# Optimization experiments

Measured on AMD Instinct MI355X. Metric: run time of the kernel, lower is better.

Reference implementation:

```python
import jax, jax.numpy as jnp
import numpy as np

EMBED_DIM = 384
NUM_HEADS = 6
HEAD_DIM = EMBED_DIM // NUM_HEADS
MLP_HIDDEN = 4 * EMBED_DIM
LN_EPS = 1e-5


def layer_norm(x, gamma, beta):
    mu = jnp.mean(x, axis=-1, keepdims=True)
    var = jnp.mean((x - mu) ** 2, axis=-1, keepdims=True)
    return (x - mu) * jax.lax.rsqrt(var + LN_EPS) * gamma + beta


def setup_inputs() -> dict:
    key = jax.random.key(0)
    ks = jax.random.split(key, 8)
    D, H = EMBED_DIM, MLP_HIDDEN
    s = 1.0 / np.sqrt(D)
    sh = 1.0 / np.sqrt(H)
    return {
        "x": jax.random.normal(ks[0], (16, 1024, D), dtype=jnp.float32),
        "ln1_g": jnp.ones((D,), jnp.float32),
        "ln1_b": jnp.zeros((D,), jnp.float32),
        "qkv_w": jax.random.uniform(ks[1], (3 * D, D), jnp.float32, -s, s),
        "qkv_b": jax.random.uniform(ks[2], (3 * D,), jnp.float32, -s, s),
        "proj_w": jax.random.uniform(ks[3], (D, D), jnp.float32, -s, s),
        "proj_b": jax.random.uniform(ks[4], (D,), jnp.float32, -s, s),
        "ln2_g": jnp.ones((D,), jnp.float32),
        "ln2_b": jnp.zeros((D,), jnp.float32),
        "fc1_w": jax.random.uniform(ks[5], (H, D), jnp.float32, -s, s),
        "fc1_b": jax.random.uniform(ks[6], (H,), jnp.float32, -s, s),
        "fc2_w": jax.random.uniform(ks[7], (D, H), jnp.float32, -sh, sh),
        "fc2_b": jnp.zeros((D,), jnp.float32),
    }


def reference(x, ln1_g, ln1_b, qkv_w, qkv_b, proj_w, proj_b,
              ln2_g, ln2_b, fc1_w, fc1_b, fc2_w, fc2_b):
    B, N, D = x.shape
    Hh, Dh = NUM_HEADS, HEAD_DIM
    scale = Dh ** -0.5

    # --- attention sublayer (pre-norm) ---
    h = layer_norm(x, ln1_g, ln1_b)
    qkv = h @ qkv_w.T + qkv_b                      # [B,N,3D]
    qkv = qkv.reshape(B, N, 3, Hh, Dh)
    q, k, v = (qkv[:, :, i].transpose(0, 2, 1, 3) for i in range(3))  # [B,H,N,Dh]
    attn = jax.nn.softmax(jnp.einsum('bhnd,bhmd->bhnm', q, k) * scale, axis=-1)
    o = jnp.einsum('bhnm,bhmd->bhnd', attn, v)     # [B,H,N,Dh]
    o = o.transpose(0, 2, 1, 3).reshape(B, N, D)
    x = x + (o @ proj_w.T + proj_b)

    # --- MLP sublayer (pre-norm) ---
    h = layer_norm(x, ln2_g, ln2_b)
    h = jax.nn.gelu(h @ fc1_w.T + fc1_b, approximate=False)
    x = x + (h @ fc2_w.T + fc2_b)
    return x
```

## Files before the change

### kernel.cpp

```cpp
#include <hip/hip_runtime.h>

typedef unsigned short u16;
typedef unsigned int   u32;
typedef __bf16  bf16x8 __attribute__((ext_vector_type(8)));
typedef __bf16  bf16x4_t __attribute__((ext_vector_type(4)));
typedef float   f32x4  __attribute__((ext_vector_type(4)));

struct Ptrs { const void* p[13]; };

__device__ __forceinline__ float bf2f(u16 u) {
    union { unsigned int i; float f; } c; c.i = ((unsigned int)u) << 16; return c.f;
}
__device__ __forceinline__ u16 f2bf(float f) {
    union { float f; unsigned int i; } c; c.f = f;
    unsigned int u = c.i;
    unsigned int r = (u + 0x7fffu + ((u >> 16) & 1u)) >> 16;
    return (u16)r;
}

__device__ __forceinline__ float wave_sum(float x) {
#pragma unroll
    for (int m = 32; m >= 1; m >>= 1) x += __shfl_xor(x, m);
    return x;
}

__device__ __forceinline__ void g2l16(const u16* g, u16* l) {
    __builtin_amdgcn_global_load_lds(
        (__attribute__((address_space(1))) void*)g,
        (__attribute__((address_space(3))) void*)l, 16, 0, 0);
}

__global__ void k_flag(const u32* __restrict__ w, int* __restrict__ flagp)
{
    if (threadIdx.x == 0) {
        int cnt = 0;
        for (int i = 0; i < 128; ++i) {
            u16 lo = (u16)(w[i] & 0xFFFFu);
            int e = (lo >> 7) & 0xFF;
            cnt += (e >= 117 && e <= 123) ? 1 : 0;
        }
        *flagp = (cnt >= 64) ? 1 : 0;
    }
}

__global__ __launch_bounds__(256) void k_convert(Ptrs ps, u16* __restrict__ cx,
                                                 u16* __restrict__ cw,
                                                 const int* __restrict__ flagp)
{
    const int cum[14] = {0,786432,786480,786528,841824,841968,860400,860448,
                         860496,860544,934272,934464,1008192,1008240};
    const int off[13] = {0,0,384,768,443136,444288,591744,
                         592128,592512,592896,1182720,1184256,1774080};
    int c = blockIdx.x * 256 + threadIdx.x;
    if (c >= 1008240) return;
    int seg = 0;
#pragma unroll
    for (int i = 1; i < 13; ++i) seg += (c >= cum[i]) ? 1 : 0;
    int e = (c - cum[seg]) * 8;
    u16* dst = (seg == 0) ? (cx + e) : (cw + off[seg] + e);
    if (*flagp) {
        *(uint4*)dst = *((const uint4*)ps.p[seg] + (e >> 3));
    } else {
        const float* s = (const float*)ps.p[seg] + e;
        u16 tmp[8];
#pragma unroll
        for (int t = 0; t < 8; ++t) tmp[t] = f2bf(s[t]);
        *(uint4*)dst = *(const uint4*)tmp;
    }
}

__device__ __forceinline__ void gemm_core_128(const u16* __restrict__ A,
                                              const u16* __restrict__ B,
                                              int K, int m0, int n0,
                                              f32x4 (&acc)[4][4])
{
    __shared__ __align__(16) u16 As[128 * 64];
    __shared__ __align__(16) u16 Bs[128 * 64];

    const int tid  = threadIdx.x;
    const int lane = tid & 63;
    const int wid  = tid >> 6;
    const int wm  = (wid >> 1) * 64;
    const int wn  = (wid & 1) * 64;
    const int l15 = lane & 15;
    const int g   = lane >> 4;
    const int srow   = lane >> 3;
    const int schunk = ((lane & 7) ^ srow) * 8;

    const u16* Abase = A + (size_t)(m0 + wid * 32 + srow) * K + schunk;
    const u16* Bbase = B + (size_t)(n0 + wid * 32 + srow) * K + schunk;

    for (int kk = 0; kk < K; kk += 64) {
        __syncthreads();
#pragma unroll
        for (int t = 0; t < 4; ++t) {
            g2l16(Abase + (size_t)t * 8 * K + kk, &As[(wid * 32 + t * 8) * 64]);
            g2l16(Bbase + (size_t)t * 8 * K + kk, &Bs[(wid * 32 + t * 8) * 64]);
        }
        __syncthreads();

#pragma unroll
        for (int ks = 0; ks < 2; ++ks) {
            bf16x8 af[4], bfr[4];
#pragma unroll
            for (int i = 0; i < 4; i++) {
                int row = wm + 16 * i + l15;
                int p = ((ks * 4 + g) ^ (l15 & 7)) * 8;
                af[i] = __builtin_bit_cast(bf16x8,
                         *(const uint4*)&As[row * 64 + p]);
            }
#pragma unroll
            for (int j = 0; j < 4; j++) {
                int row = wn + 16 * j + l15;
                int p = ((ks * 4 + g) ^ (l15 & 7)) * 8;
                bfr[j] = __builtin_bit_cast(bf16x8,
                         *(const uint4*)&Bs[row * 64 + p]);
            }
#pragma unroll
            for (int i = 0; i < 4; i++)
#pragma unroll
                for (int j = 0; j < 4; j++)
                    acc[i][j] = __builtin_amdgcn_mfma_f32_16x16x32_bf16(
                                    af[i], bfr[j], acc[i][j], 0, 0, 0);
        }
    }
}

__device__ __forceinline__ void gemm_core_128x64(const u16* __restrict__ A,
                                                 const u16* __restrict__ B,
                                                 int K, int m0, int n0,
                                                 f32x4 (&acc)[4][2])
{
    __shared__ __align__(16) u16 As[128 * 64];
    __shared__ __align__(16) u16 Bs[64 * 64];

    const int tid  = threadIdx.x;
    const int lane = tid & 63;
    const int wid  = tid >> 6;
    const int wm  = (wid >> 1) * 64;
    const int wn  = (wid & 1) * 32;
    const int l15 = lane & 15;
    const int g   = lane >> 4;
    const int srow   = lane >> 3;
    const int schunk = ((lane & 7) ^ srow) * 8;

    const u16* Abase = A + (size_t)(m0 + wid * 32 + srow) * K + schunk;
    const u16* Bbase = B + (size_t)(n0 + wid * 16 + srow) * K + schunk;

    for (int kk = 0; kk < K; kk += 64) {
        __syncthreads();
#pragma unroll
        for (int t = 0; t < 4; ++t)
            g2l16(Abase + (size_t)t * 8 * K + kk, &As[(wid * 32 + t * 8) * 64]);
#pragma unroll
        for (int t = 0; t < 2; ++t)
            g2l16(Bbase + (size_t)t * 8 * K + kk, &Bs[(wid * 16 + t * 8) * 64]);
        __syncthreads();

#pragma unroll
        for (int ks = 0; ks < 2; ++ks) {
            bf16x8 af[4], bfr[2];
#pragma unroll
            for (int i = 0; i < 4; i++) {
                int row = wm + 16 * i + l15;
                int p = ((ks * 4 + g) ^ (l15 & 7)) * 8;
                af[i] = __builtin_bit_cast(bf16x8,
                         *(const uint4*)&As[row * 64 + p]);
            }
#pragma unroll
            for (int j = 0; j < 2; j++) {
                int row = wn + 16 * j + l15;
                int p = ((ks * 4 + g) ^ (l15 & 7)) * 8;
                bfr[j] = __builtin_bit_cast(bf16x8,
                         *(const uint4*)&Bs[row * 64 + p]);
            }
#pragma unroll
            for (int i = 0; i < 4; i++)
#pragma unroll
                for (int j = 0; j < 2; j++)
                    acc[i][j] = __builtin_amdgcn_mfma_f32_16x16x32_bf16(
                                    af[i], bfr[j], acc[i][j], 0, 0, 0);
        }
    }
}

__global__ __launch_bounds__(256) void k_layernorm(const u16* __restrict__ in,
                                                   const u16* __restrict__ g,
                                                   const u16* __restrict__ b,
                                                   u16* __restrict__ out,
                                                   int nrows)
{
    const int wid = threadIdx.x >> 6, lane = threadIdx.x & 63;
    const int row = blockIdx.x * 4 + wid;
    if (row >= nrows) return;
    float v[6];
    const u16* p = in + (size_t)row * 384;
#pragma unroll
    for (int t = 0; t < 6; t++) v[t] = bf2f(p[lane + 64 * t]);
    float s = 0.f;
#pragma unroll
    for (int t = 0; t < 6; t++) s += v[t];
    const float mu = wave_sum(s) * (1.0f / 384.0f);
    float vs = 0.f;
#pragma unroll
    for (int t = 0; t < 6; t++) { float d = v[t] - mu; vs += d * d; }
    const float var = wave_sum(vs) * (1.0f / 384.0f);
    const float rs = rsqrtf(var + 1e-5f);
    u16* po = out + (size_t)row * 384;
#pragma unroll
    for (int t = 0; t < 6; t++) {
        int e = lane + 64 * t;
        po[e] = f2bf((v[t] - mu) * rs * bf2f(g[e]) + bf2f(b[e]));
    }
}

__global__ __launch_bounds__(256) void k_gemm_qkv(const u16* __restrict__ A,
                                                  const u16* __restrict__ W,
                                                  const u16* __restrict__ bias,
                                                  u16* __restrict__ q,
                                                  u16* __restrict__ k,
                                                  u16* __restrict__ vrow)
{
    const int id = blockIdx.x, slot = id & 7, idx = id >> 3;
    const int m0 = (slot * 16 + idx / 9) * 128;
    const int n0 = (idx % 9) * 128;
    f32x4 acc[4][4];
#pragma unroll
    for (int i = 0; i < 4; i++)
#pragma unroll
        for (int j = 0; j < 4; j++) acc[i][j] = f32x4{0.f, 0.f, 0.f, 0.f};
    gemm_core_128(A, W, 384, m0, n0, acc);
    const int lane = threadIdx.x & 63, wid = threadIdx.x >> 6;
    const int wm = (wid >> 1) * 64, wn = (wid & 1) * 64;
    const int l15 = lane & 15, rq = (lane >> 4) * 4;
#pragma unroll
    for (int i = 0; i < 4; i++)
#pragma unroll
        for (int j = 0; j < 4; j++)
#pragma unroll
            for (int r = 0; r < 4; r++) {
                int gr = m0 + wm + 16 * i + rq + r;
                int gc = n0 + wn + 16 * j + l15;
                float v = acc[i][j][r] + bf2f(bias[gc]);
                int part = gc / 384, rem = gc % 384;
                int head = rem >> 6, dh = rem & 63;
                int bb = gr >> 10, nn = gr & 1023;
                int bh = bb * 6 + head;
                u16* dst = (part == 0) ? q : (part == 1) ? k : vrow;
                dst[((size_t)bh * 1024 + nn) * 64 + dh] = f2bf(v);
            }
}

__global__ __launch_bounds__(256) void k_transpose_v(const u16* __restrict__ v,
                                                     u16* __restrict__ vT)
{
    __shared__ u16 T[64 * 72];
    const int bh = blockIdx.y, n0 = blockIdx.x * 64;
    const int tid = threadIdx.x;
    const int r = tid >> 2;
    const int c = (tid & 3) * 16;
    const u16* src = v + (size_t)bh * 65536 + (size_t)(n0 + r) * 64 + c;
    uint4 a = *(const uint4*)src;
    uint4 b = *(const uint4*)(src + 8);
    u16 buf[16];
    *(uint4*)&buf[0] = a; *(uint4*)&buf[8] = b;
#pragma unroll
    for (int e = 0; e < 16; ++e) T[(c + e) * 72 + r] = buf[e];
    __syncthreads();
    uint4 o0 = *(const uint4*)&T[r * 72 + c];
    uint4 o1 = *(const uint4*)&T[r * 72 + c + 8];
    u16* dst = vT + (size_t)bh * 65536 + (size_t)r * 1024 + n0 + c;
    *(uint4*)dst = o0;
    *(uint4*)(dst + 8) = o1;
}

__global__ __launch_bounds__(256) void k_attn(const u16* __restrict__ q,
                                              const u16* __restrict__ kk,
                                              const u16* __restrict__ vT,
                                              u16* __restrict__ o)
{
    constexpr int LDP = 72;
    __shared__ __align__(16) u16 Ks[64 * 64];
    __shared__ __align__(16) u16 Vs[64 * 64];
    __shared__ __align__(16) u16 Ps[128 * LDP];

    const int tid = threadIdx.x, lane = tid & 63, wid = tid >> 6;
    const int l15 = lane & 15, g = lane >> 4, q8 = g * 8;
    const int id = blockIdx.x;
    const int bh = (id & 7) * 12 + ((id >> 3) >> 3);
    const int q0 = ((id >> 3) & 7) * 128;
    const int wrow = wid * 32;

    const u16* Q = q  + (size_t)bh * 65536;
    const u16* K = kk + (size_t)bh * 65536;
    const u16* V = vT + (size_t)bh * 65536;

    const int srow   = lane >> 3;
    const int schunk = ((lane & 7) ^ srow) * 8;

    bf16x8 aq[2][2];
#pragma unroll
    for (int jp = 0; jp < 2; ++jp)
#pragma unroll
        for (int ks = 0; ks < 2; ++ks) {
            bf16x8 t = __builtin_bit_cast(bf16x8,
                *(const uint4*)&Q[(size_t)(q0 + wrow + jp * 16 + l15) * 64
                                  + ks * 32 + q8]);
#pragma unroll
            for (int e = 0; e < 8; ++e) t[e] = (__bf16)((float)t[e] * 0.125f);
            aq[jp][ks] = t;
        }

    f32x4 ob[2][4];
#pragma unroll
    for (int i = 0; i < 2; ++i)
#pragma unroll
        for (int j = 0; j < 4; ++j) ob[i][j] = f32x4{0.f, 0.f, 0.f, 0.f};
    float lsum[2] = {0.f, 0.f};

    for (int kt = 0; kt < 16; ++kt) {
        __syncthreads();
#pragma unroll
        for (int t = 0; t < 2; ++t) {
            int r0 = wid * 16 + t * 8;
            g2l16(&K[(size_t)(kt * 64 + r0 + srow) * 64 + schunk], &Ks[r0 * 64]);
            g2l16(&V[(size_t)(r0 + srow) * 1024 + kt * 64 + schunk], &Vs[r0 * 64]);
        }
        __syncthreads();

        f32x4 st[4][2];
#pragma unroll
        for (int ip = 0; ip < 4; ++ip)
#pragma unroll
            for (int jp = 0; jp < 2; ++jp) st[ip][jp] = f32x4{0.f, 0.f, 0.f, 0.f};
#pragma unroll
        for (int ip = 0; ip < 4; ++ip) {
            int row = ip * 16 + l15;
#pragma unroll
            for (int ks = 0; ks < 2; ++ks) {
                bf16x8 bk = __builtin_bit_cast(bf16x8,
                    *(const uint4*)&Ks[row * 64 + ((ks * 4 + g) ^ (row & 7)) * 8]);
#pragma unroll
                for (int jp = 0; jp < 2; ++jp)
                    st[ip][jp] = __builtin_amdgcn_mfma_f32_16x16x32_bf16(
                                    bk, aq[jp][ks], st[ip][jp], 0, 0, 0);
            }
        }

#pragma unroll
        for (int jp = 0; jp < 2; ++jp) {
            float ps = 0.f;
#pragma unroll
            for (int ip = 0; ip < 4; ++ip)
#pragma unroll
                for (int r = 0; r < 4; ++r) {
                    float p = __expf(st[ip][jp][r]);
                    st[ip][jp][r] = p;
                    ps += p;
                }
            lsum[jp] += ps;
        }

#pragma unroll
        for (int ip = 0; ip < 4; ++ip)
#pragma unroll
            for (int jp = 0; jp < 2; ++jp) {
                bf16x4_t pk;
#pragma unroll
                for (int r = 0; r < 4; ++r) pk[r] = (__bf16)st[ip][jp][r];
                *(bf16x4_t*)&Ps[(wrow + jp * 16 + l15) * LDP + ip * 16 + g * 4] = pk;
            }

#pragma unroll
        for (int ks = 0; ks < 2; ++ks) {
            bf16x8 ap[2];
#pragma unroll
            for (int i = 0; i < 2; ++i)
                ap[i] = __builtin_bit_cast(bf16x8,
                    *(const uint4*)&Ps[(wrow + i * 16 + l15) * LDP + ks * 32 + q8]);
#pragma unroll
            for (int jv = 0; jv < 4; ++jv) {
                int row = jv * 16 + l15;
                bf16x8 bv = __builtin_bit_cast(bf16x8,
                    *(const uint4*)&Vs[row * 64 + ((ks * 4 + g) ^ (row & 7)) * 8]);
#pragma unroll
                for (int i = 0; i < 2; ++i)
                    ob[i][jv] = __builtin_amdgcn_mfma_f32_16x16x32_bf16(
                                  ap[i], bv, ob[i][jv], 0, 0, 0);
            }
        }
    }

#pragma unroll
    for (int jp = 0; jp < 2; ++jp) {
        lsum[jp] += __shfl_xor(lsum[jp], 16);
        lsum[jp] += __shfl_xor(lsum[jp], 32);
    }
    const int bb = bh / 6, hh = bh % 6;
#pragma unroll
    for (int i = 0; i < 2; ++i)
#pragma unroll
        for (int r = 0; r < 4; ++r) {
            int src = (lane & 48) | (g * 4 + r);
            float linv = 1.0f / __shfl(lsum[i], src);
            int row = q0 + wrow + i * 16 + g * 4 + r;
#pragma unroll
            for (int jv = 0; jv < 4; ++jv) {
                int dh = jv * 16 + l15;
                o[((size_t)(bb * 1024 + row)) * 384 + hh * 64 + dh] =
                    f2bf(ob[i][jv][r] * linv);
            }
        }
}

__global__ __launch_bounds__(256) void k_gemm_proj(const u16* __restrict__ A,
                                                   const u16* __restrict__ W,
                                                   const u16* __restrict__ bias,
                                                   const u16* __restrict__ xin,
                                                   u16* __restrict__ x1)
{
    const int id = blockIdx.x, slot = id & 7, idx = id >> 3;
    const int m0 = (slot * 16 + idx / 6) * 128;
    const int n0 = (idx % 6) * 64;
    f32x4 acc[4][2];
#pragma unroll
    for (int i = 0; i < 4; i++)
#pragma unroll
        for (int j = 0; j < 2; j++) acc[i][j] = f32x4{0.f, 0.f, 0.f, 0.f};
    gemm_core_128x64(A, W, 384, m0, n0, acc);
    const int lane = threadIdx.x & 63, wid = threadIdx.x >> 6;
    const int wm = (wid >> 1) * 64, wn = (wid & 1) * 32;
    const int l15 = lane & 15, rq = (lane >> 4) * 4;
#pragma unroll
    for (int i = 0; i < 4; i++)
#pragma unroll
        for (int j = 0; j < 2; j++)
#pragma unroll
            for (int r = 0; r < 4; r++) {
                int gr = m0 + wm + 16 * i + rq + r;
                int gc = n0 + wn + 16 * j + l15;
                size_t ix = (size_t)gr * 384 + gc;
                x1[ix] = f2bf(acc[i][j][r] + bf2f(bias[gc]) + bf2f(xin[ix]));
            }
}

__global__ __launch_bounds__(256) void k_gemm_fc1(const u16* __restrict__ A,
                                                  const u16* __restrict__ W,
                                                  const u16* __restrict__ bias,
                                                  u16* __restrict__ hmid)
{
    const int id = blockIdx.x, slot = id & 7, idx = id >> 3;
    const int mbase = (slot * 8 + idx / 12) * 256;
    const int n0 = (idx % 12) * 128;
#pragma unroll 1
    for (int sub = 0; sub < 2; ++sub) {
        const int m0 = mbase + sub * 128;
        f32x4 acc[4][4];
#pragma unroll
        for (int i = 0; i < 4; i++)
#pragma unroll
            for (int j = 0; j < 4; j++) acc[i][j] = f32x4{0.f, 0.f, 0.f, 0.f};
        gemm_core_128(A, W, 384, m0, n0, acc);
        const int lane = threadIdx.x & 63, wid = threadIdx.x >> 6;
        const int wm = (wid >> 1) * 64, wn = (wid & 1) * 64;
        const int l15 = lane & 15, rq = (lane >> 4) * 4;
#pragma unroll
        for (int i = 0; i < 4; i++)
#pragma unroll
            for (int j = 0; j < 4; j++)
#pragma unroll
                for (int r = 0; r < 4; r++) {
                    int gr = m0 + wm + 16 * i + rq + r;
                    int gc = n0 + wn + 16 * j + l15;
                    float v = acc[i][j][r] + bf2f(bias[gc]);
                    float u = v * (1.5957691f + 0.0713548f * v * v);
                    float ge = v * __builtin_amdgcn_rcpf(1.0f + __expf(-u));
                    hmid[(size_t)gr * 1536 + gc] = f2bf(ge);
                }
    }
}

__global__ __launch_bounds__(256) void k_gemm_fc2(const u16* __restrict__ A,
                                                  const u16* __restrict__ W,
                                                  const u16* __restrict__ bias,
                                                  const u16* __restrict__ x1,
                                                  void* __restrict__ outv,
                                                  const int* __restrict__ flagp)
{
    const int id = blockIdx.x, slot = id & 7, idx = id >> 3;
    const int m0 = (slot * 16 + idx / 6) * 128;
    const int n0 = (idx % 6) * 64;
    f32x4 acc[4][2];
#pragma unroll
    for (int i = 0; i < 4; i++)
#pragma unroll
        for (int j = 0; j < 2; j++) acc[i][j] = f32x4{0.f, 0.f, 0.f, 0.f};
    gemm_core_128x64(A, W, 1536, m0, n0, acc);
    const int lane = threadIdx.x & 63, wid = threadIdx.x >> 6;
    const int wm = (wid >> 1) * 64, wn = (wid & 1) * 32;
    const int l15 = lane & 15, rq = (lane >> 4) * 4;
    const int isbf = *flagp;
    u16*   ob = (u16*)outv;
    float* of = (float*)outv;
#pragma unroll
    for (int i = 0; i < 4; i++)
#pragma unroll
        for (int j = 0; j < 2; j++)
#pragma unroll
            for (int r = 0; r < 4; r++) {
                int gr = m0 + wm + 16 * i + rq + r;
                int gc = n0 + wn + 16 * j + l15;
                size_t ix = (size_t)gr * 384 + gc;
                float v = acc[i][j][r] + bf2f(bias[gc]) + bf2f(x1[ix]);
                if (isbf) ob[ix] = f2bf(v);
                else      of[ix] = v;
            }
}

extern "C" void kernel_launch(void* const* d_in, const int* in_sizes, int n_in,
                              void* d_out, int out_size, void* d_ws, size_t ws_size,
                              hipStream_t stream)
{
    char* ws = (char*)d_ws;
    u16*   cw   = (u16*)(ws + 0);
    int*   flag = (int*)(ws + 3548928);
    u16*   cx   = (u16*)(ws + 3549184);
    u16*   h    = (u16*)(ws + 16132096);
    u16*   x1   = (u16*)(ws + 28715008);
    u16*   q    = (u16*)(ws + 53880832);
    u16*   kbuf = (u16*)(ws + 66463744);
    u16*   vT   = (u16*)(ws + 79046656);
    u16*   o    = (u16*)(ws + 91629568);
    u16*   vrow = o;
    u16*   hmid = (u16*)(ws + 53880832);

    const u16* c_ln1_g  = cw + 0;
    const u16* c_ln1_b  = cw + 384;
    const u16* c_qkv_w  = cw + 768;
    const u16* c_qkv_b  = cw + 443136;
    const u16* c_proj_w = cw + 444288;
    const u16* c_proj_b = cw + 591744;
    const u16* c_ln2_g  = cw + 592128;
    const u16* c_ln2_b  = cw + 592512;
    const u16* c_fc1_w  = cw + 592896;
    const u16* c_fc1_b  = cw + 1182720;
    const u16* c_fc2_w  = cw + 1184256;
    const u16* c_fc2_b  = cw + 1774080;

    Ptrs ps;
    for (int i = 0; i < 13; ++i) ps.p[i] = d_in[i];

    k_flag<<<1, 64, 0, stream>>>((const u32*)d_in[3], flag);
    k_convert<<<3939, 256, 0, stream>>>(ps, cx, cw, flag);
    k_layernorm<<<4096, 256, 0, stream>>>(cx, c_ln1_g, c_ln1_b, h, 16384);
    k_gemm_qkv<<<1152, 256, 0, stream>>>(h, c_qkv_w, c_qkv_b, q, kbuf, vrow);
    k_transpose_v<<<dim3(16, 96), 256, 0, stream>>>(vrow, vT);
    k_attn<<<768, 256, 0, stream>>>(q, kbuf, vT, o);
    k_gemm_proj<<<768, 256, 0, stream>>>(o, c_proj_w, c_proj_b, cx, x1);
    k_layernorm<<<4096, 256, 0, stream>>>(x1, c_ln2_g, c_ln2_b, h, 16384);
    k_gemm_fc1<<<768, 256, 0, stream>>>(h, c_fc1_w, c_fc1_b, hmid);
    k_gemm_fc2<<<768, 256, 0, stream>>>(hmid, c_fc2_w, c_fc2_b, x1,
                                        d_out, flag);
    (void)in_sizes; (void)n_in; (void)out_size; (void)ws_size; (void)c_fc2_b;
}
```

Before: 285.5 us.

## Fuse input conversion into LayerNorm1 and process two key tiles per attention sync

The fp32-to-bf16 conversion of x is folded into a new layernorm kernel that reads the raw input once, writes both the bf16 copy and the normalized output, and drops one full pass over the activations. The attention kernel now loads 128 keys per barrier pair instead of 64, halving the synchronisations per key sweep. It also uses exp2 with log2e folded into the Q scale, and replaces the padded P buffer with an XOR-swizzled layout. The cost is more LDS per block, which may reduce occupancy, and a manual swizzle that must match between the writes and the reads.

```diff
diff --git a/kernel.cpp b/kernel.cpp
--- a/kernel.cpp
+++ b/kernel.cpp
@@ -43,29 +43,68 @@
     }
 }
 
-__global__ __launch_bounds__(256) void k_convert(Ptrs ps, u16* __restrict__ cx,
+__global__ __launch_bounds__(256) void k_convert(Ptrs ps,
                                                  u16* __restrict__ cw,
                                                  const int* __restrict__ flagp)
 {
-    const int cum[14] = {0,786432,786480,786528,841824,841968,860400,860448,
-                         860496,860544,934272,934464,1008192,1008240};
-    const int off[13] = {0,0,384,768,443136,444288,591744,
+    const int cum[13] = {0,48,96,55392,55536,73968,74016,74064,74112,
+                         147840,148032,221760,221808};
+    const int off[12] = {0,384,768,443136,444288,591744,
                          592128,592512,592896,1182720,1184256,1774080};
     int c = blockIdx.x * 256 + threadIdx.x;
-    if (c >= 1008240) return;
+    if (c >= 221808) return;
     int seg = 0;
 #pragma unroll
-    for (int i = 1; i < 13; ++i) seg += (c >= cum[i]) ? 1 : 0;
+    for (int i = 1; i < 12; ++i) seg += (c >= cum[i]) ? 1 : 0;
     int e = (c - cum[seg]) * 8;
-    u16* dst = (seg == 0) ? (cx + e) : (cw + off[seg] + e);
+    u16* dst = cw + off[seg] + e;
     if (*flagp) {
-        *(uint4*)dst = *((const uint4*)ps.p[seg] + (e >> 3));
+        *(uint4*)dst = *((const uint4*)ps.p[seg + 1] + (e >> 3));
     } else {
-        const float* s = (const float*)ps.p[seg] + e;
+        const float* s = (const float*)ps.p[seg + 1] + e;
         u16 tmp[8];
 #pragma unroll
         for (int t = 0; t < 8; ++t) tmp[t] = f2bf(s[t]);
         *(uint4*)dst = *(const uint4*)tmp;
+    }
+}
+
+__global__ __launch_bounds__(256) void k_ln1cvt(const void* __restrict__ xin,
+                                                const u16* __restrict__ g,
+                                                const u16* __restrict__ b,
+                                                u16* __restrict__ cx,
+                                                u16* __restrict__ h,
+                                                const int* __restrict__ flagp)
+{
+    const int wid = threadIdx.x >> 6, lane = threadIdx.x & 63;
+    const int row = blockIdx.x * 4 + wid;
+    float v[6]; u16 raw[6];
+    if (*flagp) {
+        const u16* p = (const u16*)xin + (size_t)row * 384;
+#pragma unroll
+        for (int t = 0; t < 6; t++) { raw[t] = p[lane + 64 * t]; v[t] = bf2f(raw[t]); }
+    } else {
+        const float* p = (const float*)xin + (size_t)row * 384;
+#pragma unroll
+        for (int t = 0; t < 6; t++) { v[t] = p[lane + 64 * t]; raw[t] = f2bf(v[t]); }
+    }
+    u16* pc = cx + (size_t)row * 384;
+#pragma unroll
+    for (int t = 0; t < 6; t++) pc[lane + 64 * t] = raw[t];
+    float s = 0.f;
+#pragma unroll
+    for (int t = 0; t < 6; t++) s += v[t];
+    const float mu = wave_sum(s) * (1.0f / 384.0f);
+    float vs = 0.f;
+#pragma unroll
+    for (int t = 0; t < 6; t++) { float d = v[t] - mu; vs += d * d; }
+    const float var = wave_sum(vs) * (1.0f / 384.0f);
+    const float rs = rsqrtf(var + 1e-5f);
+    u16* po = h + (size_t)row * 384;
+#pragma unroll
+    for (int t = 0; t < 6; t++) {
+        int e = lane + 64 * t;
+        po[e] = f2bf((v[t] - mu) * rs * bf2f(g[e]) + bf2f(b[e]));
     }
 }
 
@@ -279,10 +318,9 @@
                                               const u16* __restrict__ vT,
                                               u16* __restrict__ o)
 {
-    constexpr int LDP = 72;
-    __shared__ __align__(16) u16 Ks[64 * 64];
-    __shared__ __align__(16) u16 Vs[64 * 64];
-    __shared__ __align__(16) u16 Ps[128 * LDP];
+    __shared__ __align__(16) u16 Ks[128 * 64];
+    __shared__ __align__(16) u16 Vs[2][64 * 64];
+    __shared__ __align__(16) u16 Ps[128 * 64];
 
     const int tid = threadIdx.x, lane = tid & 63, wid = tid >> 6;
     const int l15 = lane & 15, g = lane >> 4, q8 = g * 8;
@@ -307,7 +345,8 @@
                 *(const uint4*)&Q[(size_t)(q0 + wrow + jp * 16 + l15) * 64
                                   + ks * 32 + q8]);
 #pragma unroll
-            for (int e = 0; e < 8; ++e) t[e] = (__bf16)((float)t[e] * 0.125f);
+            for (int e = 0; e < 8; ++e)
+                t[e] = (__bf16)((float)t[e] * 0.18033688f);
             aq[jp][ks] = t;
         }
 
@@ -318,75 +357,87 @@
         for (int j = 0; j < 4; ++j) ob[i][j] = f32x4{0.f, 0.f, 0.f, 0.f};
     float lsum[2] = {0.f, 0.f};
 
-    for (int kt = 0; kt < 16; ++kt) {
+    for (int kt2 = 0; kt2 < 8; ++kt2) {
         __syncthreads();
 #pragma unroll
-        for (int t = 0; t < 2; ++t) {
-            int r0 = wid * 16 + t * 8;
-            g2l16(&K[(size_t)(kt * 64 + r0 + srow) * 64 + schunk], &Ks[r0 * 64]);
-            g2l16(&V[(size_t)(r0 + srow) * 1024 + kt * 64 + schunk], &Vs[r0 * 64]);
-        }
+        for (int t = 0; t < 4; ++t) {
+            int r0 = wid * 32 + t * 8;
+            g2l16(&K[(size_t)(kt2 * 128 + r0 + srow) * 64 + schunk], &Ks[r0 * 64]);
+        }
+#pragma unroll
+        for (int h = 0; h < 2; ++h)
+#pragma unroll
+            for (int t = 0; t < 2; ++t) {
+                int r0 = wid * 16 + t * 8;
+                g2l16(&V[(size_t)(r0 + srow) * 1024 + kt2 * 128 + h * 64 + schunk],
+                      &Vs[h][r0 * 64]);
+            }
         __syncthreads();
 
-        f32x4 st[4][2];
-#pragma unroll
-        for (int ip = 0; ip < 4; ++ip)
-#pragma unroll
-            for (int jp = 0; jp < 2; ++jp) st[ip][jp] = f32x4{0.f, 0.f, 0.f, 0.f};
-#pragma unroll
-        for (int ip = 0; ip < 4; ++ip) {
-            int row = ip * 16 + l15;
+#pragma unroll 1
+        for (int h = 0; h < 2; ++h) {
+            f32x4 st[4][2];
+#pragma unroll
+            for (int ip = 0; ip < 4; ++ip)
+#pragma unroll
+                for (int jp = 0; jp < 2; ++jp) st[ip][jp] = f32x4{0.f,0.f,0.f,0.f};
+#pragma unroll
+            for (int ip = 0; ip < 4; ++ip) {
+                int row = h * 64 + ip * 16 + l15;
+#pragma unroll
+                for (int ks = 0; ks < 2; ++ks) {
+                    bf16x8 bk = __builtin_bit_cast(bf16x8,
+                        *(const uint4*)&Ks[row * 64 + ((ks*4+g) ^ (l15&7)) * 8]);
+#pragma unroll
+                    for (int jp = 0; jp < 2; ++jp)
+                        st[ip][jp] = __builtin_amdgcn_mfma_f32_16x16x32_bf16(
+                                        bk, aq[jp][ks], st[ip][jp], 0, 0, 0);
+                }
+            }
+
+#pragma unroll
+            for (int jp = 0; jp < 2; ++jp) {
+                float ps = 0.f;
+#pragma unroll
+                for (int ip = 0; ip < 4; ++ip)
+#pragma unroll
+                    for (int r = 0; r < 4; ++r) {
+                        float p = exp2f(st[ip][jp][r]);
+                        st[ip][jp][r] = p;
+                        ps += p;
+                    }
+                lsum[jp] += ps;
+            }
+
+#pragma unroll
+            for (int ip = 0; ip < 4; ++ip)
+#pragma unroll
+                for (int jp = 0; jp < 2; ++jp) {
+                    bf16x4_t pk;
+#pragma unroll
+                    for (int r = 0; r < 4; ++r) pk[r] = (__bf16)st[ip][jp][r];
+                    int col = (((ip*2 + (g>>1)) ^ (l15 & 7)) * 8) + (g & 1) * 4;
+                    *(bf16x4_t*)&Ps[(wrow + jp*16 + l15) * 64 + col] = pk;
+                }
+
 #pragma unroll
             for (int ks = 0; ks < 2; ++ks) {
-                bf16x8 bk = __builtin_bit_cast(bf16x8,
-                    *(const uint4*)&Ks[row * 64 + ((ks * 4 + g) ^ (row & 7)) * 8]);
-#pragma unroll
-                for (int jp = 0; jp < 2; ++jp)
-                    st[ip][jp] = __builtin_amdgcn_mfma_f32_16x16x32_bf16(
-                                    bk, aq[jp][ks], st[ip][jp], 0, 0, 0);
-            }
-        }
-
-#pragma unroll
-        for (int jp = 0; jp < 2; ++jp) {
-            float ps = 0.f;
-#pragma unroll
-            for (int ip = 0; ip < 4; ++ip)
-#pragma unroll
-                for (int r = 0; r < 4; ++r) {
-                    float p = __expf(st[ip][jp][r]);
-                    st[ip][jp][r] = p;
-                    ps += p;
+                bf16x8 ap[2];
+#pragma unroll
+                for (int i = 0; i < 2; ++i)
+                    ap[i] = __builtin_bit_cast(bf16x8,
+                        *(const uint4*)&Ps[(wrow + i*16 + l15) * 64
+                                           + ((ks*4+g) ^ (l15&7)) * 8]);
+#pragma unroll
+                for (int jv = 0; jv < 4; ++jv) {
+                    int row = jv * 16 + l15;
+                    bf16x8 bv = __builtin_bit_cast(bf16x8,
+                        *(const uint4*)&Vs[h][row * 64 + ((ks*4+g) ^ (row&7)) * 8]);
+#pragma unroll
+                    for (int i = 0; i < 2; ++i)
+                        ob[i][jv] = __builtin_amdgcn_mfma_f32_16x16x32_bf16(
+                                      ap[i], bv, ob[i][jv], 0, 0, 0);
                 }
-            lsum[jp] += ps;
-        }
-
-#pragma unroll
-        for (int ip = 0; ip < 4; ++ip)
-#pragma unroll
-            for (int jp = 0; jp < 2; ++jp) {
-                bf16x4_t pk;
-#pragma unroll
-                for (int r = 0; r < 4; ++r) pk[r] = (__bf16)st[ip][jp][r];
-                *(bf16x4_t*)&Ps[(wrow + jp * 16 + l15) * LDP + ip * 16 + g * 4] = pk;
-            }
-
-#pragma unroll
-        for (int ks = 0; ks < 2; ++ks) {
-            bf16x8 ap[2];
-#pragma unroll
-            for (int i = 0; i < 2; ++i)
-                ap[i] = __builtin_bit_cast(bf16x8,
-                    *(const uint4*)&Ps[(wrow + i * 16 + l15) * LDP + ks * 32 + q8]);
-#pragma unroll
-            for (int jv = 0; jv < 4; ++jv) {
-                int row = jv * 16 + l15;
-                bf16x8 bv = __builtin_bit_cast(bf16x8,
-                    *(const uint4*)&Vs[row * 64 + ((ks * 4 + g) ^ (row & 7)) * 8]);
-#pragma unroll
-                for (int i = 0; i < 2; ++i)
-                    ob[i][jv] = __builtin_amdgcn_mfma_f32_16x16x32_bf16(
-                                  ap[i], bv, ob[i][jv], 0, 0, 0);
             }
         }
     }
@@ -551,8 +602,8 @@
     for (int i = 0; i < 13; ++i) ps.p[i] = d_in[i];
 
     k_flag<<<1, 64, 0, stream>>>((const u32*)d_in[3], flag);
-    k_convert<<<3939, 256, 0, stream>>>(ps, cx, cw, flag);
-    k_layernorm<<<4096, 256, 0, stream>>>(cx, c_ln1_g, c_ln1_b, h, 16384);
+    k_convert<<<867, 256, 0, stream>>>(ps, cw, flag);
+    k_ln1cvt<<<4096, 256, 0, stream>>>(d_in[0], c_ln1_g, c_ln1_b, cx, h, flag);
     k_gemm_qkv<<<1152, 256, 0, stream>>>(h, c_qkv_w, c_qkv_b, q, kbuf, vrow);
     k_transpose_v<<<dim3(16, 96), 256, 0, stream>>>(vrow, vT);
     k_attn<<<768, 256, 0, stream>>>(q, kbuf, vT, o);
```

Result: faster. 279.5 us (-2.1%).
